# Performance work log

Measured on AMD Instinct MI355X. Metric: run time of the kernel, lower is better.

## Reference

```python
import jax, jax.numpy as jnp
import numpy as np

B, S, IN, H, BB, M = 256, 512, 64, 256, 256, 64


def _lecun_tanh(x):
    return 1.7159 * jnp.tanh(0.666 * x)


def setup_inputs() -> dict:
    key = jax.random.key(0)
    ks = jax.random.split(key, 32)
    def g(i, shape, fan_in):
        return jax.random.normal(ks[i], shape, jnp.float32) * (fan_in ** -0.5)
    return {
        "x": jax.random.normal(ks[0], (B, S, IN), jnp.float32),
        "timespans": jax.random.uniform(ks[1], (B, S), jnp.float32, minval=0.01, maxval=1.0),
        "hx": jnp.zeros((B, H), jnp.float32),
        # CfC cell backbone (2 layers, lecun_tanh)
        "bb_w0": g(2, (IN + H, BB), IN + H), "bb_b0": jnp.zeros((BB,), jnp.float32),
        "bb_w1": g(3, (BB, BB), BB), "bb_b1": jnp.zeros((BB,), jnp.float32),
        # CfC heads ff1/ff2/time_a/time_b
        "ff1_w": g(4, (BB, H), BB), "ff1_b": jnp.zeros((H,), jnp.float32),
        "ff2_w": g(5, (BB, H), BB), "ff2_b": jnp.zeros((H,), jnp.float32),
        "ta_w": g(6, (BB, H), BB), "ta_b": jnp.zeros((H,), jnp.float32),
        "tb_w": g(7, (BB, H), BB), "tb_b": jnp.zeros((H,), jnp.float32),
        # projection hidden -> motor
        "proj_w": g(8, (H, M), H), "proj_b": jnp.zeros((M,), jnp.float32),
        # intensity head: M->16 SiLU ->3 Softplus
        "ih_w0": g(9, (M, 16), M), "ih_b0": jnp.zeros((16,), jnp.float32),
        "ih_w1": g(10, (16, 3), 16), "ih_b1": jnp.zeros((3,), jnp.float32),
        # action head: M->16 SiLU ->1 Tanh
        "ah_w0": g(11, (M, 16), M), "ah_b0": jnp.zeros((16,), jnp.float32),
        "ah_w1": g(12, (16, 1), 16), "ah_b1": jnp.zeros((1,), jnp.float32),
        # confidence head: M->8 SiLU ->1 Sigmoid
        "ch_w0": g(13, (M, 8), M), "ch_b0": jnp.zeros((8,), jnp.float32),
        "ch_w1": g(14, (8, 1), 8), "ch_b1": jnp.zeros((1,), jnp.float32),
    }


def reference(x, timespans, hx, bb_w0, bb_b0, bb_w1, bb_b1, ff1_w, ff1_b, ff2_w, ff2_b,
              ta_w, ta_b, tb_w, tb_b, proj_w, proj_b,
              ih_w0, ih_b0, ih_w1, ih_b1, ah_w0, ah_b0, ah_w1, ah_b1,
              ch_w0, ch_b0, ch_w1, ch_b1):
    ts = timespans[..., None]  # (B,S,1)

    def step(h, inp):
        x_t, ts_t = inp  # (B,IN), (B,1)
        z = jnp.concatenate([x_t, h], axis=-1)
        z = _lecun_tanh(z @ bb_w0 + bb_b0)
        z = _lecun_tanh(z @ bb_w1 + bb_b1)
        ff1 = jnp.tanh(z @ ff1_w + ff1_b)
        ff2 = jnp.tanh(z @ ff2_w + ff2_b)
        t_interp = jax.nn.sigmoid((z @ ta_w + ta_b) * ts_t + (z @ tb_w + tb_b))
        h_new = ff1 * (1.0 - t_interp) + t_interp * ff2
        return h_new, h_new

    xs = (jnp.swapaxes(x, 0, 1), jnp.swapaxes(ts, 0, 1))  # time-major
    h_n, h_seq = jax.lax.scan(step, hx, xs)               # h_seq: (S,B,H)
    cfc = jnp.swapaxes(h_seq, 0, 1) @ proj_w + proj_b     # (B,S,M)
    intensities = jax.nn.softplus(jax.nn.silu(cfc @ ih_w0 + ih_b0) @ ih_w1 + ih_b1)
    actions = jnp.tanh(jax.nn.silu(cfc @ ah_w0 + ah_b0) @ ah_w1 + ah_b1)
    confidence = jax.nn.sigmoid(jax.nn.silu(cfc @ ch_w0 + ch_b0) @ ch_w1 + ch_b1)
    return intensities, actions, confidence, h_n
```

## Files before the change

### kernel.cpp

```cpp
#include <hip/hip_runtime.h>
#include <hip/hip_bf16.h>

#define BN  256
#define SN  512
#define INN 64
#define HN  256
#define MN  64

#define ZINS 328
#define ZBS  264
#define CFS  72
#define HTS  36

#define OFF_ACT  393216
#define OFF_CONF 524288
#define OFF_HN   655360

#define HBUF_OFF 16384
#define HBUF_BYTES (2 * 256 * 64 * 8)

typedef _Float16 h8 __attribute__((ext_vector_type(8)));
typedef float fx4 __attribute__((ext_vector_type(4)));
typedef unsigned long long u64;
union h4u { _Float16 h[4]; unsigned short s[4]; u64 u; };

__device__ __forceinline__ fx4 mfma16(h8 a, h8 b, fx4 c) {
    return __builtin_amdgcn_mfma_f32_16x16x32_f16(a, b, c, 0, 0, 0);
}
__device__ __forceinline__ float fast_tanh(float x) {
    float e = __expf(2.0f * x);
    return 1.0f - 2.0f / (e + 1.0f);
}
__device__ __forceinline__ float fast_sig(float x) { return 1.0f / (1.0f + __expf(-x)); }
__device__ __forceinline__ float lecun_tanh(float x) { return 1.7159f * fast_tanh(0.666f * x); }
__device__ __forceinline__ float softplus_f(float x) {
    return fmaxf(x, 0.0f) + __logf(1.0f + __expf(-fabsf(x)));
}

template <int NW>
__device__ __forceinline__ h8 loadB(const float* __restrict__ w, int col, int kbase) {
    h8 r;
#pragma unroll
    for (int j = 0; j < 8; ++j) r[j] = (_Float16)w[(kbase + j) * NW + col];
    return r;
}

__global__ void __launch_bounds__(512, 1) lh_scan_kernel(
    const float* __restrict__ x, const float* __restrict__ tsp, const float* __restrict__ hx,
    const float* __restrict__ w0, const float* __restrict__ b0,
    const float* __restrict__ w1, const float* __restrict__ b1,
    const float* __restrict__ f1w, const float* __restrict__ f1b,
    const float* __restrict__ f2w, const float* __restrict__ f2b,
    const float* __restrict__ taw, const float* __restrict__ tab,
    const float* __restrict__ tbw, const float* __restrict__ tbb,
    const float* __restrict__ pw, const float* __restrict__ pbias,
    const float* __restrict__ ihw0, const float* __restrict__ ihb0,
    const float* __restrict__ ihw1, const float* __restrict__ ihb1,
    const float* __restrict__ ahw0, const float* __restrict__ ahb0,
    const float* __restrict__ ahw1, const float* __restrict__ ahb1,
    const float* __restrict__ chw0, const float* __restrict__ chb0,
    const float* __restrict__ chw1, const float* __restrict__ chb1,
    float* __restrict__ out, u64* __restrict__ hbuf)
{
    __shared__ __align__(16) _Float16 zin[16 * ZINS];
    __shared__ __align__(16) _Float16 z0b[16 * ZBS];
    __shared__ __align__(16) _Float16 z1b[16 * ZBS];
    __shared__ __align__(16) _Float16 cfcb[16 * CFS];
    __shared__ __align__(16) _Float16 pfl[8 * 4 * 64 * 8];
    __shared__ __align__(16) _Float16 w1l[8 * 8 * 64 * 8];
    __shared__ __align__(16) float htmp[4 * 16 * HTS];
    __shared__ float hidI[16 * 16];
    __shared__ float hidA[16 * 16];
    __shared__ float hidC[16 * 8];
    __shared__ float tsb[2][16];
    __shared__ float wsm[80];

    const int tid  = threadIdx.x;
    const int wv   = tid >> 6;
    const int lane = tid & 63;
    const int lo   = lane & 15;
    const int hi   = lane >> 4;
    const int hi8  = hi * 8;

    const int bid   = blockIdx.x;
    const int xcd   = bid & 7;
    const int c     = (bid >> 3) & 7;
    const int gsel  = bid >> 6;
    const int g     = xcd + 8 * gsel;
    const int bg    = g * 16;
    const int sbase = c * 32;

    if (tid < 48)          wsm[tid] = ihw1[tid];
    else if (tid < 51)     wsm[tid] = ihb1[tid - 48];
    else if (tid < 67)     wsm[tid] = ahw1[tid - 51];
    else if (tid == 67)    wsm[67]  = ahb1[0];
    else if (tid < 76)     wsm[tid] = chw1[tid - 68];
    else if (tid == 76)    wsm[76]  = chb1[0];

    {
        int r = tid >> 5, c8 = (tid & 31) * 8;
#pragma unroll
        for (int j = 0; j < 8; ++j)
            zin[r * ZINS + 64 + c8 + j] = (_Float16)hx[(bg + r) * HN + c8 + j];
        int c2 = (tid & 31) * 2;
        const float* xp = &x[((size_t)(bg + r) * SN + 0) * INN + c2];
        zin[r * ZINS + c2]     = (_Float16)xp[0];
        zin[r * ZINS + c2 + 1] = (_Float16)xp[1];
    }
    if (tid < 16) tsb[0][tid] = tsp[(bg + tid) * SN + 0];

    const int cg0 = wv, cg1 = wv + 8;
    const float b00 = b0[cg0 * 16 + lo], b01 = b0[cg1 * 16 + lo];
    const float b10 = b1[cg0 * 16 + lo], b11 = b1[cg1 * 16 + lo];

    const int hm   = wv >> 1;
    const int hcol = sbase + (wv & 1) * 16 + lo;
    const float* hwp = (hm == 0) ? f1w : (hm == 1) ? f2w : (hm == 2) ? taw : tbw;
    const float* hbp = (hm == 0) ? f1b : (hm == 1) ? f2b : (hm == 2) ? tab : tbb;
    const float hb = hbp[hcol];

    h8 w0f0[10], w0f1[10], w1f0[8], hdf[8];
#pragma unroll
    for (int kk = 0; kk < 10; ++kk) {
        w0f0[kk] = loadB<256>(w0, cg0 * 16 + lo, kk * 32 + hi8);
        w0f1[kk] = loadB<256>(w0, cg1 * 16 + lo, kk * 32 + hi8);
    }
#pragma unroll
    for (int kk = 0; kk < 8; ++kk) {
        w1f0[kk] = loadB<256>(w1, cg0 * 16 + lo, kk * 32 + hi8);
        hdf[kk]  = loadB<256>(hwp, hcol, kk * 32 + hi8);
        h8 f = loadB<256>(w1, cg1 * 16 + lo, kk * 32 + hi8);
        *(h8*)&w1l[((kk * 8 + wv) * 64 + lane) * 8] = f;
    }
    float pbv = 0.0f;
    if (wv < 4) {
        pbv = pbias[wv * 16 + lo];
#pragma unroll
        for (int kk = 0; kk < 8; ++kk) {
            h8 f = loadB<64>(pw, wv * 16 + lo, kk * 32 + hi8);
            *(h8*)&pfl[((kk * 4 + wv) * 64 + lane) * 8] = f;
        }
    }
    h8 hwf[2] = {};
    float hbv = 0.0f;
    if (wv == 4) {
        hbv = ihb0[lo];
#pragma unroll
        for (int kk = 0; kk < 2; ++kk) hwf[kk] = loadB<16>(ihw0, lo, kk * 32 + hi8);
    } else if (wv == 5) {
        hbv = ahb0[lo];
#pragma unroll
        for (int kk = 0; kk < 2; ++kk) hwf[kk] = loadB<16>(ahw0, lo, kk * 32 + hi8);
    } else if (wv == 6) {
        int cc = (lo < 8) ? lo : 0;
        hbv = (lo < 8) ? chb0[lo] : 0.0f;
#pragma unroll
        for (int kk = 0; kk < 2; ++kk) hwf[kk] = loadB<8>(chw0, cc, kk * 32 + hi8);
    }

    __syncthreads();

    for (int t = 0; t <= SN; ++t) {
        const int pr = t & 7;
        const unsigned tagc = ((((unsigned)(t + 1)) >> 1) + 1u) & 3u;

        if (t < SN) {
            fx4 a0 = {b00, b00, b00, b00}, a1 = {b01, b01, b01, b01};
#pragma unroll
            for (int kk = 0; kk < 10; ++kk) {
                h8 a = *(const h8*)&zin[lo * ZINS + kk * 32 + hi8];
                a0 = mfma16(a, w0f0[kk], a0);
                a1 = mfma16(a, w0f1[kk], a1);
            }
#pragma unroll
            for (int i = 0; i < 4; ++i) {
                int r = hi * 4 + i;
                z0b[r * ZBS + cg0 * 16 + lo] = (_Float16)lecun_tanh(a0[i]);
                z0b[r * ZBS + cg1 * 16 + lo] = (_Float16)lecun_tanh(a1[i]);
            }
        }
        __syncthreads();

        if (t + 1 < SN) {
            int r = tid >> 5, c2 = (tid & 31) * 2;
            const float* xp = &x[((size_t)(bg + r) * SN + (t + 1)) * INN + c2];
            zin[r * ZINS + c2]     = (_Float16)xp[0];
            zin[r * ZINS + c2 + 1] = (_Float16)xp[1];
            if (tid < 16) tsb[(t + 1) & 1][tid] = tsp[(bg + tid) * SN + t + 1];
        }

        if (t < SN) {
            fx4 a0 = {b10, b10, b10, b10}, a1 = {b11, b11, b11, b11};
#pragma unroll
            for (int kk = 0; kk < 8; ++kk) {
                h8 a = *(const h8*)&z0b[lo * ZBS + kk * 32 + hi8];
                h8 bf = *(const h8*)&w1l[((kk * 8 + wv) * 64 + lane) * 8];
                a0 = mfma16(a, w1f0[kk], a0);
                a1 = mfma16(a, bf, a1);
            }
#pragma unroll
            for (int i = 0; i < 4; ++i) {
                int r = hi * 4 + i;
                z1b[r * ZBS + cg0 * 16 + lo] = (_Float16)lecun_tanh(a0[i]);
                z1b[r * ZBS + cg1 * 16 + lo] = (_Float16)lecun_tanh(a1[i]);
            }
        }
        __syncthreads();

        if (t < SN) {
            fx4 acc = {hb, hb, hb, hb};
#pragma unroll
            for (int kk = 0; kk < 8; ++kk) {
                h8 a = *(const h8*)&z1b[lo * ZBS + kk * 32 + hi8];
                acc = mfma16(a, hdf[kk], acc);
            }
#pragma unroll
            for (int i = 0; i < 4; ++i)
                htmp[(hm * 16 + hi * 4 + i) * HTS + (wv & 1) * 16 + lo] = acc[i];
        }
        __syncthreads();

        if (t < SN && tid < 128) {
            int r = tid >> 3, c4 = (tid & 7) * 4;
            h4u pk;
            float tv = tsb[t & 1][r];
#pragma unroll
            for (int k = 0; k < 4; ++k) {
                float a1v = htmp[(0 * 16 + r) * HTS + c4 + k];
                float a2v = htmp[(1 * 16 + r) * HTS + c4 + k];
                float a3v = htmp[(2 * 16 + r) * HTS + c4 + k];
                float a4v = htmp[(3 * 16 + r) * HTS + c4 + k];
                float ff1 = fast_tanh(a1v);
                float ff2 = fast_tanh(a2v);
                float ti  = fast_sig(a3v * tv + a4v);
                float hn  = ff1 + ti * (ff2 - ff1);
                pk.h[k] = (_Float16)hn;
                unsigned tb = (k & 1) ? ((tagc >> 1) & 1u) : (tagc & 1u);
                pk.s[k] = (unsigned short)((pk.s[k] & 0xFFFEu) | tb);
                if (t == SN - 1) out[OFF_HN + (bg + r) * HN + sbase + c4 + k] = hn;
            }
            size_t idx = (((size_t)((t + 1) & 1) * 256) + g * 16 + r) * 64 + (sbase + c4) / 4;
            __hip_atomic_store(&hbuf[idx], pk.u, __ATOMIC_RELAXED, __HIP_MEMORY_SCOPE_AGENT);
        }
        __syncthreads();

        if (t >= 1 && c == pr && wv < 4) {
            fx4 acc = {pbv, pbv, pbv, pbv};
#pragma unroll
            for (int kk = 0; kk < 8; ++kk) {
                h8 a = *(const h8*)&zin[lo * ZINS + 64 + kk * 32 + hi8];
                h8 b = *(const h8*)&pfl[((kk * 4 + wv) * 64 + lane) * 8];
                acc = mfma16(a, b, acc);
            }
#pragma unroll
            for (int i = 0; i < 4; ++i)
                cfcb[(hi * 4 + i) * CFS + wv * 16 + lo] = (_Float16)acc[i];
        }
        __syncthreads();

        if (t >= 1 && c == pr && wv >= 4 && wv < 7) {
            fx4 acc = {hbv, hbv, hbv, hbv};
#pragma unroll
            for (int kk = 0; kk < 2; ++kk) {
                h8 a = *(const h8*)&cfcb[lo * CFS + kk * 32 + hi8];
                acc = mfma16(a, hwf[kk], acc);
            }
#pragma unroll
            for (int i = 0; i < 4; ++i) {
                float v = acc[i];
                v = v * fast_sig(v);
                int r = hi * 4 + i;
                if (wv == 4)       hidI[r * 16 + lo] = v;
                else if (wv == 5)  hidA[r * 16 + lo] = v;
                else if (lo < 8)   hidC[r * 8 + lo]  = v;
            }
        }
        __syncthreads();

        if (t >= 1 && c == pr && tid < 80) {
            int r = tid / 5, o = tid % 5;
            int tc = t - 1;
            int b = bg + r;
            if (o < 3) {
                float s = wsm[48 + o];
#pragma unroll
                for (int u = 0; u < 16; ++u) s += hidI[r * 16 + u] * wsm[u * 3 + o];
                out[(size_t)(b * SN + tc) * 3 + o] = softplus_f(s);
            } else if (o == 3) {
                float s = wsm[67];
#pragma unroll
                for (int u = 0; u < 16; ++u) s += hidA[r * 16 + u] * wsm[51 + u];
                out[OFF_ACT + b * SN + tc] = fast_tanh(s);
            } else {
                float s = wsm[76];
#pragma unroll
                for (int u = 0; u < 8; ++u) s += hidC[r * 8 + u] * wsm[68 + u];
                out[OFF_CONF + b * SN + tc] = fast_sig(s);
            }
        }

        if (t < SN) {
            int r = tid >> 5, c8 = (tid & 31) * 8;
            size_t idx = (((size_t)((t + 1) & 1) * 256) + g * 16 + r) * 64 + c8 / 4;
            const unsigned b0e = tagc & 1u, b1e = (tagc >> 1) & 1u;
            u64 v0 = __hip_atomic_load(&hbuf[idx],     __ATOMIC_RELAXED, __HIP_MEMORY_SCOPE_AGENT);
            u64 v1 = __hip_atomic_load(&hbuf[idx + 1], __ATOMIC_RELAXED, __HIP_MEMORY_SCOPE_AGENT);
            while ((unsigned)(v0 & 1u) != b0e || (unsigned)((v0 >> 16) & 1u) != b1e)
                v0 = __hip_atomic_load(&hbuf[idx],     __ATOMIC_RELAXED, __HIP_MEMORY_SCOPE_AGENT);
            while ((unsigned)(v1 & 1u) != b0e || (unsigned)((v1 >> 16) & 1u) != b1e)
                v1 = __hip_atomic_load(&hbuf[idx + 1], __ATOMIC_RELAXED, __HIP_MEMORY_SCOPE_AGENT);
            *(u64*)&zin[r * ZINS + 64 + c8]     = v0;
            *(u64*)&zin[r * ZINS + 64 + c8 + 4] = v1;
        }
        __syncthreads();
    }
}

extern "C" void kernel_launch(void* const* d_in, const int* in_sizes, int n_in,
                              void* d_out, int out_size, void* d_ws, size_t ws_size,
                              hipStream_t stream) {
    (void)in_sizes; (void)n_in; (void)out_size; (void)ws_size;
    const float* p[29];
    for (int i = 0; i < 29; ++i) p[i] = (const float*)d_in[i];
    u64* hbuf = (u64*)((char*)d_ws + HBUF_OFF);
    hipMemsetAsync(hbuf, 0xAA, HBUF_BYTES, stream);
    hipLaunchKernelGGL(lh_scan_kernel, dim3(128), dim3(512), 0, stream,
        p[0], p[1], p[2], p[3], p[4], p[5], p[6], p[7], p[8], p[9], p[10], p[11], p[12],
        p[13], p[14], p[15], p[16], p[17], p[18], p[19], p[20], p[21], p[22], p[23],
        p[24], p[25], p[26], p[27], p[28], (float*)d_out, hbuf);
}
```

Measured before the change: 2.390 ms.

## Read peer hidden state straight from global flags into MFMA operands, drop barriers

Workgroups no longer copy the exchanged hidden state from the global tag-flagged buffer into shared memory behind a dedicated spin-and-barrier phase. Each wave issues the tagged atomic loads early, runs the x-part of the first matmul while they are in flight, then spins per fragment and feeds the values directly to MFMA. The projection stage reads the same buffer directly, which removes two __syncthreads per step. The initial hx is written into the buffer with tags, and the head-wave assignment is remapped. The cost is redundant global loads per wave and subtler tag and parity reasoning about when buffer slots may be overwritten.

```diff
diff --git a/kernel.cpp b/kernel.cpp
--- a/kernel.cpp
+++ b/kernel.cpp
@@ -7,7 +7,7 @@
 #define HN  256
 #define MN  64
 
-#define ZINS 328
+#define ZXS  72
 #define ZBS  264
 #define CFS  72
 #define HTS  36
@@ -16,13 +16,14 @@
 #define OFF_CONF 524288
 #define OFF_HN   655360
 
-#define HBUF_OFF 16384
-#define HBUF_BYTES (2 * 256 * 64 * 8)
+#define HBUF_U64_SLOT 16384ull
+#define HBUF_BYTES    (2 * 16384 * 8)
 
 typedef _Float16 h8 __attribute__((ext_vector_type(8)));
 typedef float fx4 __attribute__((ext_vector_type(4)));
 typedef unsigned long long u64;
 union h4u { _Float16 h[4]; unsigned short s[4]; u64 u; };
+union h8u { u64 u[2]; h8 v; };
 
 __device__ __forceinline__ fx4 mfma16(h8 a, h8 b, fx4 c) {
     return __builtin_amdgcn_mfma_f32_16x16x32_f16(a, b, c, 0, 0, 0);
@@ -35,6 +36,9 @@
 __device__ __forceinline__ float lecun_tanh(float x) { return 1.7159f * fast_tanh(0.666f * x); }
 __device__ __forceinline__ float softplus_f(float x) {
     return fmaxf(x, 0.0f) + __logf(1.0f + __expf(-fabsf(x)));
+}
+__device__ __forceinline__ bool tagok(u64 v, unsigned b0e, unsigned b1e) {
+    return (((unsigned)v & 1u) == b0e) && ((((unsigned)(v >> 16)) & 1u) == b1e);
 }
 
 template <int NW>
@@ -62,7 +66,7 @@
     const float* __restrict__ chw1, const float* __restrict__ chb1,
     float* __restrict__ out, u64* __restrict__ hbuf)
 {
-    __shared__ __align__(16) _Float16 zin[16 * ZINS];
+    __shared__ __align__(16) _Float16 zinx[16 * ZXS];
     __shared__ __align__(16) _Float16 z0b[16 * ZBS];
     __shared__ __align__(16) _Float16 z1b[16 * ZBS];
     __shared__ __align__(16) _Float16 cfcb[16 * CFS];
@@ -98,14 +102,22 @@
     else if (tid == 76)    wsm[76]  = chb1[0];
 
     {
-        int r = tid >> 5, c8 = (tid & 31) * 8;
-#pragma unroll
-        for (int j = 0; j < 8; ++j)
-            zin[r * ZINS + 64 + c8 + j] = (_Float16)hx[(bg + r) * HN + c8 + j];
-        int c2 = (tid & 31) * 2;
+        int r = tid >> 5, c2 = (tid & 31) * 2;
         const float* xp = &x[((size_t)(bg + r) * SN + 0) * INN + c2];
-        zin[r * ZINS + c2]     = (_Float16)xp[0];
-        zin[r * ZINS + c2 + 1] = (_Float16)xp[1];
+        zinx[r * ZXS + c2]     = (_Float16)xp[0];
+        zinx[r * ZXS + c2 + 1] = (_Float16)xp[1];
+    }
+    if (tid < 128) {
+        int r = tid >> 3, c4 = (tid & 7) * 4;
+        h4u pk;
+#pragma unroll
+        for (int k = 0; k < 4; ++k) {
+            pk.h[k] = (_Float16)hx[(bg + r) * HN + sbase + c4 + k];
+            unsigned tb = (k & 1) ? 0u : 1u;
+            pk.s[k] = (unsigned short)((pk.s[k] & 0xFFFEu) | tb);
+        }
+        size_t idx = (size_t)(g * 16 + r) * 64 + (sbase + c4) / 4;
+        __hip_atomic_store(&hbuf[idx], pk.u, __ATOMIC_RELAXED, __HIP_MEMORY_SCOPE_AGENT);
     }
     if (tid < 16) tsb[0][tid] = tsp[(bg + tid) * SN + 0];
 
@@ -132,26 +144,26 @@
         h8 f = loadB<256>(w1, cg1 * 16 + lo, kk * 32 + hi8);
         *(h8*)&w1l[((kk * 8 + wv) * 64 + lane) * 8] = f;
     }
-    float pbv = 0.0f;
     if (wv < 4) {
-        pbv = pbias[wv * 16 + lo];
 #pragma unroll
         for (int kk = 0; kk < 8; ++kk) {
             h8 f = loadB<64>(pw, wv * 16 + lo, kk * 32 + hi8);
             *(h8*)&pfl[((kk * 4 + wv) * 64 + lane) * 8] = f;
         }
     }
+    float pbv = 0.0f;
+    if (wv >= 2 && wv < 6) pbv = pbias[(wv - 2) * 16 + lo];
     h8 hwf[2] = {};
     float hbv = 0.0f;
-    if (wv == 4) {
+    if (wv == 2) {
         hbv = ihb0[lo];
 #pragma unroll
         for (int kk = 0; kk < 2; ++kk) hwf[kk] = loadB<16>(ihw0, lo, kk * 32 + hi8);
-    } else if (wv == 5) {
+    } else if (wv == 3) {
         hbv = ahb0[lo];
 #pragma unroll
         for (int kk = 0; kk < 2; ++kk) hwf[kk] = loadB<16>(ahw0, lo, kk * 32 + hi8);
-    } else if (wv == 6) {
+    } else if (wv == 4) {
         int cc = (lo < 8) ? lo : 0;
         hbv = (lo < 8) ? chb0[lo] : 0.0f;
 #pragma unroll
@@ -162,15 +174,34 @@
 
     for (int t = 0; t <= SN; ++t) {
         const int pr = t & 7;
-        const unsigned tagc = ((((unsigned)(t + 1)) >> 1) + 1u) & 3u;
+        const unsigned tagL = (((unsigned)t >> 1) + 1u) & 3u;
+        const unsigned b0e = tagL & 1u, b1e = (tagL >> 1) & 1u;
+        const unsigned tagP = ((((unsigned)(t + 1)) >> 1) + 1u) & 3u;
+        const size_t hbL = (size_t)(t & 1) * HBUF_U64_SLOT + (size_t)(g * 16 + lo) * 64 + hi * 2;
 
         if (t < SN) {
+            u64 r0[8], r1[8];
+#pragma unroll
+            for (int s = 0; s < 8; ++s) {
+                r0[s] = __hip_atomic_load(&hbuf[hbL + s * 8],     __ATOMIC_RELAXED, __HIP_MEMORY_SCOPE_AGENT);
+                r1[s] = __hip_atomic_load(&hbuf[hbL + s * 8 + 1], __ATOMIC_RELAXED, __HIP_MEMORY_SCOPE_AGENT);
+            }
             fx4 a0 = {b00, b00, b00, b00}, a1 = {b01, b01, b01, b01};
-#pragma unroll
-            for (int kk = 0; kk < 10; ++kk) {
-                h8 a = *(const h8*)&zin[lo * ZINS + kk * 32 + hi8];
-                a0 = mfma16(a, w0f0[kk], a0);
-                a1 = mfma16(a, w0f1[kk], a1);
+            {
+                h8 ax0 = *(const h8*)&zinx[lo * ZXS + hi8];
+                h8 ax1 = *(const h8*)&zinx[lo * ZXS + 32 + hi8];
+                a0 = mfma16(ax0, w0f0[0], a0); a1 = mfma16(ax0, w0f1[0], a1);
+                a0 = mfma16(ax1, w0f0[1], a0); a1 = mfma16(ax1, w0f1[1], a1);
+            }
+#pragma unroll
+            for (int s = 0; s < 8; ++s) {
+                while (!tagok(r0[s], b0e, b1e))
+                    r0[s] = __hip_atomic_load(&hbuf[hbL + s * 8],     __ATOMIC_RELAXED, __HIP_MEMORY_SCOPE_AGENT);
+                while (!tagok(r1[s], b0e, b1e))
+                    r1[s] = __hip_atomic_load(&hbuf[hbL + s * 8 + 1], __ATOMIC_RELAXED, __HIP_MEMORY_SCOPE_AGENT);
+                h8u f; f.u[0] = r0[s]; f.u[1] = r1[s];
+                a0 = mfma16(f.v, w0f0[s + 2], a0);
+                a1 = mfma16(f.v, w0f1[s + 2], a1);
             }
 #pragma unroll
             for (int i = 0; i < 4; ++i) {
@@ -184,16 +215,15 @@
         if (t + 1 < SN) {
             int r = tid >> 5, c2 = (tid & 31) * 2;
             const float* xp = &x[((size_t)(bg + r) * SN + (t + 1)) * INN + c2];
-            zin[r * ZINS + c2]     = (_Float16)xp[0];
-            zin[r * ZINS + c2 + 1] = (_Float16)xp[1];
+            zinx[r * ZXS + c2]     = (_Float16)xp[0];
+            zinx[r * ZXS + c2 + 1] = (_Float16)xp[1];
             if (tid < 16) tsb[(t + 1) & 1][tid] = tsp[(bg + tid) * SN + t + 1];
         }
-
         if (t < SN) {
             fx4 a0 = {b10, b10, b10, b10}, a1 = {b11, b11, b11, b11};
 #pragma unroll
             for (int kk = 0; kk < 8; ++kk) {
-                h8 a = *(const h8*)&z0b[lo * ZBS + kk * 32 + hi8];
+                h8 a  = *(const h8*)&z0b[lo * ZBS + kk * 32 + hi8];
                 h8 bf = *(const h8*)&w1l[((kk * 8 + wv) * 64 + lane) * 8];
                 a0 = mfma16(a, w1f0[kk], a0);
                 a1 = mfma16(a, bf, a1);
@@ -235,30 +265,35 @@
                 float ti  = fast_sig(a3v * tv + a4v);
                 float hn  = ff1 + ti * (ff2 - ff1);
                 pk.h[k] = (_Float16)hn;
-                unsigned tb = (k & 1) ? ((tagc >> 1) & 1u) : (tagc & 1u);
+                unsigned tb = (k & 1) ? ((tagP >> 1) & 1u) : (tagP & 1u);
                 pk.s[k] = (unsigned short)((pk.s[k] & 0xFFFEu) | tb);
                 if (t == SN - 1) out[OFF_HN + (bg + r) * HN + sbase + c4 + k] = hn;
             }
             size_t idx = (((size_t)((t + 1) & 1) * 256) + g * 16 + r) * 64 + (sbase + c4) / 4;
             __hip_atomic_store(&hbuf[idx], pk.u, __ATOMIC_RELAXED, __HIP_MEMORY_SCOPE_AGENT);
         }
-        __syncthreads();
-
-        if (t >= 1 && c == pr && wv < 4) {
+        if (t >= 1 && c == pr && wv >= 2 && wv < 6) {
+            int u = wv - 2;
             fx4 acc = {pbv, pbv, pbv, pbv};
 #pragma unroll
-            for (int kk = 0; kk < 8; ++kk) {
-                h8 a = *(const h8*)&zin[lo * ZINS + 64 + kk * 32 + hi8];
-                h8 b = *(const h8*)&pfl[((kk * 4 + wv) * 64 + lane) * 8];
-                acc = mfma16(a, b, acc);
+            for (int s = 0; s < 8; ++s) {
+                u64 v0 = __hip_atomic_load(&hbuf[hbL + s * 8],     __ATOMIC_RELAXED, __HIP_MEMORY_SCOPE_AGENT);
+                u64 v1 = __hip_atomic_load(&hbuf[hbL + s * 8 + 1], __ATOMIC_RELAXED, __HIP_MEMORY_SCOPE_AGENT);
+                while (!tagok(v0, b0e, b1e))
+                    v0 = __hip_atomic_load(&hbuf[hbL + s * 8],     __ATOMIC_RELAXED, __HIP_MEMORY_SCOPE_AGENT);
+                while (!tagok(v1, b0e, b1e))
+                    v1 = __hip_atomic_load(&hbuf[hbL + s * 8 + 1], __ATOMIC_RELAXED, __HIP_MEMORY_SCOPE_AGENT);
+                h8u f; f.u[0] = v0; f.u[1] = v1;
+                h8 b = *(const h8*)&pfl[((s * 4 + u) * 64 + lane) * 8];
+                acc = mfma16(f.v, b, acc);
             }
 #pragma unroll
             for (int i = 0; i < 4; ++i)
-                cfcb[(hi * 4 + i) * CFS + wv * 16 + lo] = (_Float16)acc[i];
-        }
-        __syncthreads();
-
-        if (t >= 1 && c == pr && wv >= 4 && wv < 7) {
+                cfcb[(hi * 4 + i) * CFS + u * 16 + lo] = (_Float16)acc[i];
+        }
+        __syncthreads();
+
+        if (t >= 1 && c == pr && wv >= 2 && wv < 5) {
             fx4 acc = {hbv, hbv, hbv, hbv};
 #pragma unroll
             for (int kk = 0; kk < 2; ++kk) {
@@ -270,8 +305,8 @@
                 float v = acc[i];
                 v = v * fast_sig(v);
                 int r = hi * 4 + i;
-                if (wv == 4)       hidI[r * 16 + lo] = v;
-                else if (wv == 5)  hidA[r * 16 + lo] = v;
+                if (wv == 2)       hidI[r * 16 + lo] = v;
+                else if (wv == 3)  hidA[r * 16 + lo] = v;
                 else if (lo < 8)   hidC[r * 8 + lo]  = v;
             }
         }
@@ -298,21 +333,6 @@
                 out[OFF_CONF + b * SN + tc] = fast_sig(s);
             }
         }
-
-        if (t < SN) {
-            int r = tid >> 5, c8 = (tid & 31) * 8;
-            size_t idx = (((size_t)((t + 1) & 1) * 256) + g * 16 + r) * 64 + c8 / 4;
-            const unsigned b0e = tagc & 1u, b1e = (tagc >> 1) & 1u;
-            u64 v0 = __hip_atomic_load(&hbuf[idx],     __ATOMIC_RELAXED, __HIP_MEMORY_SCOPE_AGENT);
-            u64 v1 = __hip_atomic_load(&hbuf[idx + 1], __ATOMIC_RELAXED, __HIP_MEMORY_SCOPE_AGENT);
-            while ((unsigned)(v0 & 1u) != b0e || (unsigned)((v0 >> 16) & 1u) != b1e)
-                v0 = __hip_atomic_load(&hbuf[idx],     __ATOMIC_RELAXED, __HIP_MEMORY_SCOPE_AGENT);
-            while ((unsigned)(v1 & 1u) != b0e || (unsigned)((v1 >> 16) & 1u) != b1e)
-                v1 = __hip_atomic_load(&hbuf[idx + 1], __ATOMIC_RELAXED, __HIP_MEMORY_SCOPE_AGENT);
-            *(u64*)&zin[r * ZINS + 64 + c8]     = v0;
-            *(u64*)&zin[r * ZINS + 64 + c8 + 4] = v1;
-        }
-        __syncthreads();
     }
 }
 
@@ -322,7 +342,7 @@
     (void)in_sizes; (void)n_in; (void)out_size; (void)ws_size;
     const float* p[29];
     for (int i = 0; i < 29; ++i) p[i] = (const float*)d_in[i];
-    u64* hbuf = (u64*)((char*)d_ws + HBUF_OFF);
+    u64* hbuf = (u64*)d_ws;
     hipMemsetAsync(hbuf, 0xAA, HBUF_BYTES, stream);
     hipLaunchKernelGGL(lh_scan_kernel, dim3(128), dim3(512), 0, stream,
         p[0], p[1], p[2], p[3], p[4], p[5], p[6], p[7], p[8], p[9], p[10], p[11], p[12],
```

New measurement: 4.258 ms. 78.1% more time.
